# Performance work log

Hardware: AMD Instinct MI355X
Metric: run time of the kernel (lower is better)

The kernel has to match this reference:

```python
import jax, jax.numpy as jnp
import numpy as np

B, T, D = 64, 512, 512
K_CODES = 256
K_FUTURE = 2


def _gru(x, w_ih, w_hh, b_ih, b_hh):
    # x: [B,T,D]; PyTorch GRU gate order: r, z, n; weights [3D, D]
    xg = jnp.einsum('btd,gd->btg', x, w_ih) + b_ih  # [B,T,3D] precomputed input gates

    def step(h, xg_t):
        hg = h @ w_hh.T + b_hh                      # [B,3D]
        xr, xz, xn = jnp.split(xg_t, 3, axis=-1)
        hr, hz, hn = jnp.split(hg, 3, axis=-1)
        r = jax.nn.sigmoid(xr + hr)
        z = jax.nn.sigmoid(xz + hz)
        n = jnp.tanh(xn + r * hn)
        h_new = (1.0 - z) * n + z * h
        return h_new, h_new

    h0 = jnp.zeros((x.shape[0], w_hh.shape[1]), x.dtype)
    _, hs = jax.lax.scan(step, h0, jnp.swapaxes(xg, 0, 1))
    return jnp.swapaxes(hs, 0, 1)  # [B,T,D]


def setup_inputs() -> dict:
    key = jax.random.key(0)
    ks = jax.random.split(key, 8)
    return {
        'features': jax.random.normal(ks[0], (B, T, D), jnp.float32),
        'codebook': jax.random.uniform(ks[1], (K_CODES, D), jnp.float32, -0.1, 0.1),
        'w_ih': jax.random.normal(ks[2], (3 * D, D), jnp.float32) * 0.02,
        'w_hh': jax.random.normal(ks[3], (3 * D, D), jnp.float32) * 0.02,
        'b_ih': jax.random.normal(ks[4], (3 * D,), jnp.float32) * 0.02,
        'b_hh': jax.random.normal(ks[5], (3 * D,), jnp.float32) * 0.02,
        'proj_w': jax.random.normal(ks[6], (D, D), jnp.float32) * 0.02,
        'proj_b': jax.random.normal(ks[7], (D,), jnp.float32) * 0.02,
    }


def reference(features, codebook, w_ih, w_hh, b_ih, b_hh, proj_w, proj_b):
    b, t, d = features.shape
    # --- quantize: cdist + argmin + gather (squared dists give same argmin) ---
    flat = features.reshape(-1, d)                              # [B*T, D]
    d2 = (jnp.sum(flat * flat, axis=1, keepdims=True)
          - 2.0 * flat @ codebook.T
          + jnp.sum(codebook * codebook, axis=1))               # [B*T, K]
    indices = jnp.argmin(d2, axis=1)                            # [B*T]
    quantized = codebook[indices].reshape(b, t, d)              # gather
    indices = indices.reshape(b, t)

    # --- context prediction loss ---
    hidden = _gru(quantized, w_ih, w_hh, b_ih, b_hh)            # [B,T,D]
    context_proj = hidden @ proj_w.T + proj_b                   # [B,T,D]
    k_max = min(K_FUTURE, t - 1)
    cp_loss = jnp.float32(0.0)
    for k in range(1, k_max + 1):
        cp_loss = cp_loss + jnp.mean((context_proj[:, :-k] - features[:, k:]) ** 2)
    cp_loss = cp_loss / k_max

    # --- VQ loss (stop_gradient mirrors torch .detach()) ---
    commitment_loss = jnp.mean((jax.lax.stop_gradient(features) - quantized) ** 2)
    codebook_loss = jnp.mean((features - jax.lax.stop_gradient(quantized)) ** 2)
    vq_loss = commitment_loss + 0.25 * codebook_loss

    total_loss = cp_loss + vq_loss
    return quantized, indices, total_loss, cp_loss, vq_loss
```

## Files before the change

### kernel.cpp

```cpp
#include <hip/hip_runtime.h>
#include <hip/hip_bf16.h>

#define B_ 64
#define T_ 512
#define D_ 512
#define K_ 256
#define G3 1536

typedef __attribute__((ext_vector_type(8))) short sh8;
typedef __attribute__((ext_vector_type(4))) short sh4;
typedef __attribute__((ext_vector_type(4))) float fx4;
typedef __attribute__((ext_vector_type(4))) int   ix4;

__device__ __forceinline__ short f2bf(float x) {
  __hip_bfloat16 h = __float2bfloat16(x);
  union { __hip_bfloat16 h; short s; } u; u.h = h; return u.s;
}
__device__ __forceinline__ float sigm(float x) { return 1.f / (1.f + __expf(-x)); }
__device__ __forceinline__ float tanh_fast(float x) {
  float e2 = __expf(-2.f * x);
  return (1.f - e2) / (1.f + e2);
}

__global__ void k_cnorm(const float* __restrict__ cb, double* __restrict__ cn) {
  int c = threadIdx.x;
  if (c < K_) {
    double s = 0.0;
    for (int k = 0; k < D_; ++k) { double v = cb[c * D_ + k]; s += v * v; }
    cn[c] = s;
  }
}

__global__ __launch_bounds__(256) void k_cg(const float* __restrict__ cb,
                                            const float* __restrict__ wih,
                                            const float* __restrict__ bih,
                                            const float* __restrict__ bhh,
                                            float* __restrict__ cg) {
  __shared__ float wl[16][512];
  int j0 = blockIdx.x * 16, c0 = blockIdx.y * 64;
  for (int v = threadIdx.x; v < 16 * 128; v += 256) {
    int r = v >> 7, q = v & 127;
    *(fx4*)&wl[r][q * 4] = *(const fx4*)&wih[(j0 + r) * D_ + q * 4];
  }
  __syncthreads();
  for (int p = threadIdx.x; p < 1024; p += 256) {
    int j = p >> 6, c = c0 + (p & 63);
    fx4 a = {0.f, 0.f, 0.f, 0.f};
    const float* cbr = &cb[c * D_];
    for (int q = 0; q < 128; ++q) {
      fx4 w4 = *(fx4*)&wl[j][q * 4];
      fx4 c4 = *(const fx4*)&cbr[q * 4];
      a += w4 * c4;
    }
    int jg = j0 + j;
    float bias = bih[jg] + (jg < 1024 ? bhh[jg] : 0.f);
    cg[c * G3 + jg] = ((a.x + a.y) + (a.z + a.w)) + bias;
  }
}

__global__ void k_cvt(const float* __restrict__ src, __hip_bfloat16* __restrict__ dst, int n4) {
  int i = blockIdx.x * blockDim.x + threadIdx.x;
  if (i < n4) {
    fx4 v = *(const fx4*)&src[i * 4];
    sh4 o; o[0] = f2bf(v.x); o[1] = f2bf(v.y); o[2] = f2bf(v.z); o[3] = f2bf(v.w);
    *(sh4*)&dst[i * 4] = o;
  }
}

__global__ __launch_bounds__(256) void k_quant(const float* __restrict__ feat,
                                               const float* __restrict__ cb,
                                               const double* __restrict__ cn,
                                               int* __restrict__ idxw,
                                               float* __restrict__ outq,
                                               float* __restrict__ outi,
                                               double* __restrict__ lacc) {
  __shared__ float fl[16][516];
  __shared__ double ss1[16][16], ss2[16][16];
  __shared__ int ii1[16][16], ii2[16][16];
  __shared__ int idxl[16];
  __shared__ float rsv[4];
  int row0 = blockIdx.x * 16;
  int tid = threadIdx.x;
  for (int v = tid; v < 16 * 128; v += 256) {
    int r = v >> 7, q = v & 127;
    *(fx4*)&fl[r][q * 4] = *(const fx4*)&feat[(row0 + r) * D_ + q * 4];
  }
  __syncthreads();
  int r = tid & 15, g = tid >> 4;
  fx4 acc[16];
#pragma unroll
  for (int c = 0; c < 16; ++c) acc[c] = (fx4){0.f, 0.f, 0.f, 0.f};
  for (int ch = 0; ch < 8; ++ch) {
    fx4 fc[16];
#pragma unroll
    for (int q = 0; q < 16; ++q) fc[q] = *(fx4*)&fl[r][ch * 64 + q * 4];
#pragma unroll
    for (int c = 0; c < 16; ++c) {
      const float* cbp = &cb[(g * 16 + c) * D_ + ch * 64];
#pragma unroll
      for (int q = 0; q < 16; ++q) {
        fx4 c4 = *(const fx4*)&cbp[q * 4];
        acc[c] += fc[q] * c4;
      }
    }
  }
  double b1 = 1e300, b2 = 1e300; int i1 = 0, i2 = 0;
#pragma unroll
  for (int c = 0; c < 16; ++c) {
    int ci = g * 16 + c;
    double dot = (double)acc[c].x + acc[c].y + acc[c].z + acc[c].w;
    double s = cn[ci] - 2.0 * dot;
    if (s < b1) { b2 = b1; i2 = i1; b1 = s; i1 = ci; }
    else if (s < b2) { b2 = s; i2 = ci; }
  }
  ss1[r][g] = b1; ss2[r][g] = b2; ii1[r][g] = i1; ii2[r][g] = i2;
  __syncthreads();
  if (tid < 16) {
    int rr = tid;
    double c1 = 1e300, c2 = 1e300; int j1 = 0, j2 = 0;
    for (int g2 = 0; g2 < 16; ++g2) {
      double s = ss1[rr][g2]; int ix = ii1[rr][g2];
      if (s < c1 || (s == c1 && ix < j1)) { c2 = c1; j2 = j1; c1 = s; j1 = ix; }
      else if (s < c2 || (s == c2 && ix < j2)) { c2 = s; j2 = ix; }
      s = ss2[rr][g2]; ix = ii2[rr][g2];
      if (s < c1 || (s == c1 && ix < j1)) { c2 = c1; j2 = j1; c1 = s; j1 = ix; }
      else if (s < c2 || (s == c2 && ix < j2)) { c2 = s; j2 = ix; }
    }
    int pick = j1;
    if (c2 - c1 < 1e-4) {
      double d1 = 0.0, d2 = 0.0;
      for (int k = 0; k < D_; ++k) {
        double fv = fl[rr][k];
        d1 += fv * (double)cb[j1 * D_ + k];
        d2 += fv * (double)cb[j2 * D_ + k];
      }
      double e1 = cn[j1] - 2.0 * d1, e2 = cn[j2] - 2.0 * d2;
      if (e2 < e1 || (e2 == e1 && j2 < j1)) pick = j2;
    }
    idxl[rr] = pick;
    idxw[row0 + rr] = pick;
    outi[row0 + rr] = (float)pick;
  }
  __syncthreads();
  float vs = 0.f;
  for (int v = tid; v < 16 * 128; v += 256) {
    int rr = v >> 7, q = v & 127;
    fx4 c4 = *(const fx4*)&cb[idxl[rr] * D_ + q * 4];
    *(fx4*)&outq[(row0 + rr) * D_ + q * 4] = c4;
    fx4 f4 = *(fx4*)&fl[rr][q * 4];
    fx4 d = f4 - c4;
    vs += d.x * d.x + d.y * d.y + d.z * d.z + d.w * d.w;
  }
#pragma unroll
  for (int off = 32; off > 0; off >>= 1) vs += __shfl_down(vs, off);
  if ((tid & 63) == 0) rsv[tid >> 6] = vs;
  __syncthreads();
  if (tid == 0) atomicAdd(&lacc[2], (double)(rsv[0] + rsv[1] + rsv[2] + rsv[3]));
}

__global__ __launch_bounds__(256, 1) void k_gru(const float* __restrict__ whh,
                                                const float* __restrict__ bhh,
                                                const float* __restrict__ cg,
                                                const int* __restrict__ idx,
                                                __hip_bfloat16* __restrict__ hid,
                                                unsigned int* __restrict__ flag,
                                                int* __restrict__ xcca,
                                                unsigned int* __restrict__ bar0) {
  int bid = blockIdx.x;
  int g = bid & 7, s = bid >> 3;
  int tid = threadIdx.x;
  int w = tid >> 6, lane = tid & 63, l15 = lane & 15, l4 = lane >> 4;
  int wv = s * 4 + w;

  sh8 A0[16], A1[16], A2[16];
#pragma unroll
  for (int kt = 0; kt < 16; ++kt) {
#pragma unroll
    for (int t3 = 0; t3 < 3; ++t3) {
      const float* wr = &whh[((t3 * 512) + s * 64 + w * 16 + l15) * D_];
      int k0 = kt * 32 + l4 * 8;
      fx4 x = *(const fx4*)&wr[k0];
      fx4 y = *(const fx4*)&wr[k0 + 4];
      sh8 tt;
      tt[0] = f2bf(x.x); tt[1] = f2bf(x.y); tt[2] = f2bf(x.z); tt[3] = f2bf(x.w);
      tt[4] = f2bf(y.x); tt[5] = f2bf(y.y); tt[6] = f2bf(y.z); tt[7] = f2bf(y.w);
      if (t3 == 0) A0[kt] = tt; else if (t3 == 1) A1[kt] = tt; else A2[kt] = tt;
    }
  }

  const bool act = (l15 < 8);
  const int b = l15 & 7;
  const int dg0 = s * 64 + w * 16 + l4 * 4;

  fx4 bn = *(const fx4*)&bhh[1024 + dg0];
  fx4 hp = {0.f, 0.f, 0.f, 0.f};

  __shared__ int sh_fast;
  if (tid == 0) {
    int xcc = 0;
    asm volatile("s_getreg_b32 %0, hwreg(HW_REG_XCC_ID)" : "=s"(xcc));
    __hip_atomic_store(&xcca[bid], xcc, __ATOMIC_RELEASE, __HIP_MEMORY_SCOPE_AGENT);
    __hip_atomic_fetch_add(bar0, 1u, __ATOMIC_ACQ_REL, __HIP_MEMORY_SCOPE_AGENT);
    while (__hip_atomic_load(bar0, __ATOMIC_ACQUIRE, __HIP_MEMORY_SCOPE_AGENT) < 64u)
      __builtin_amdgcn_s_sleep(2);
    int x0 = __hip_atomic_load(&xcca[g], __ATOMIC_RELAXED, __HIP_MEMORY_SCOPE_AGENT);
    int f = 1;
    for (int m = 1; m < 8; ++m)
      if (__hip_atomic_load(&xcca[g + 8 * m], __ATOMIC_RELAXED, __HIP_MEMORY_SCOPE_AGENT) != x0)
        f = 0;
    sh_fast = f;
    __threadfence();
  }
  __syncthreads();
  const bool fast = (sh_fast != 0);

  const unsigned* myfp = &flag[(g * 32 + (lane & 31)) * 32];

  for (int t = 0; t < T_; ++t) {
    fx4 cr = {0, 0, 0, 0}, cz = {0, 0, 0, 0}, cnn = {0, 0, 0, 0};
    if (act) {
      int ci = idx[(g * 8 + b) * T_ + t];
      const float* cgr = &cg[(size_t)ci * G3 + dg0];
      cr  = *(const fx4*)cgr;
      cz  = *(const fx4*)(cgr + 512);
      cnn = *(const fx4*)(cgr + 1024);
    }

    fx4 a0 = {0, 0, 0, 0}, a1 = {0, 0, 0, 0}, a2 = {0, 0, 0, 0};
    if (t > 0) {
      for (;;) {
        unsigned v = __hip_atomic_load(myfp, __ATOMIC_RELAXED, __HIP_MEMORY_SCOPE_AGENT);
        if (__all((int)(v >= (unsigned)t))) break;
        __builtin_amdgcn_s_sleep(1);
      }
      asm volatile("" ::: "memory");
      if (!fast) __threadfence();

      const __hip_bfloat16* hrow =
          &hid[((size_t)(g * 8 + b) * T_ + (t - 1)) * D_];
#pragma unroll
      for (int kt = 0; kt < 16; ++kt) {
        sh8 bfr = {0, 0, 0, 0, 0, 0, 0, 0};
        if (act) bfr = *(const sh8*)&hrow[kt * 32 + l4 * 8];
        a0 = __builtin_amdgcn_mfma_f32_16x16x32_bf16(A0[kt], bfr, a0, 0, 0, 0);
        a1 = __builtin_amdgcn_mfma_f32_16x16x32_bf16(A1[kt], bfr, a1, 0, 0, 0);
        a2 = __builtin_amdgcn_mfma_f32_16x16x32_bf16(A2[kt], bfr, a2, 0, 0, 0);
      }
    }

    if (act) {
      sh4 hb4;
#pragma unroll
      for (int rg = 0; rg < 4; ++rg) {
        float rr = sigm(cr[rg] + a0[rg]);
        float zz = sigm(cz[rg] + a1[rg]);
        float nn = tanh_fast(cnn[rg] + rr * (a2[rg] + bn[rg]));
        float hv = (1.f - zz) * nn + zz * hp[rg];
        hp[rg] = hv;
        hb4[rg] = f2bf(hv);
      }
      *(sh4*)&hid[((size_t)(g * 8 + b) * T_ + t) * D_ + dg0] = hb4;
    }
    asm volatile("s_waitcnt vmcnt(0)" ::: "memory");
    if (!fast) __threadfence();
    if (lane == 0)
      __hip_atomic_store(&flag[(g * 32 + wv) * 32], (unsigned)(t + 1),
                         __ATOMIC_RELAXED, __HIP_MEMORY_SCOPE_AGENT);
  }
}

__global__ __launch_bounds__(256) void k_proj(const __hip_bfloat16* __restrict__ hid,
                                              const __hip_bfloat16* __restrict__ pwb,
                                              const float* __restrict__ pb,
                                              const float* __restrict__ feat,
                                              double* __restrict__ lacc) {
  __shared__ char Bl[512 * 64];
  __shared__ char Al[32 * 64];
  __shared__ float rs1[4], rs2[4];
  int Mb = blockIdx.x * 32;
  int tid = threadIdx.x;
  int w = tid >> 6, lane = tid & 63, l15 = lane & 15, l4 = lane >> 4;
  fx4 acc[2][8];
#pragma unroll
  for (int a = 0; a < 2; ++a)
#pragma unroll
    for (int b = 0; b < 8; ++b) acc[a][b] = (fx4){0, 0, 0, 0};

  for (int kc = 0; kc < 16; ++kc) {
    for (int v = tid; v < 2048; v += 256) {
      int rw = v >> 2, sg = v & 3;
      ix4 d = *(const ix4*)&pwb[rw * D_ + kc * 32 + sg * 8];
      *(ix4*)(Bl + rw * 64 + ((sg * 16) ^ ((rw & 7) << 4))) = d;
    }
    if (tid < 128) {
      int rw = tid >> 2, sg = tid & 3;
      ix4 d = *(const ix4*)&hid[(size_t)(Mb + rw) * D_ + kc * 32 + sg * 8];
      *(ix4*)(Al + rw * 64 + ((sg * 16) ^ ((rw & 7) << 4))) = d;
    }
    __syncthreads();
    sh8 af0, af1;
    {
      int m = l15;
      af0 = *(const sh8*)(Al + m * 64 + ((l4 * 16) ^ ((m & 7) << 4)));
      m = 16 + l15;
      af1 = *(const sh8*)(Al + m * 64 + ((l4 * 16) ^ ((m & 7) << 4)));
    }
#pragma unroll
    for (int nt = 0; nt < 8; ++nt) {
      int n = (w * 8 + nt) * 16 + l15;
      sh8 bf = *(const sh8*)(Bl + n * 64 + ((l4 * 16) ^ ((n & 7) << 4)));
      acc[0][nt] = __builtin_amdgcn_mfma_f32_16x16x32_bf16(af0, bf, acc[0][nt], 0, 0, 0);
      acc[1][nt] = __builtin_amdgcn_mfma_f32_16x16x32_bf16(af1, bf, acc[1][nt], 0, 0, 0);
    }
    __syncthreads();
  }

  float s1 = 0.f, s2 = 0.f;
#pragma unroll
  for (int mt = 0; mt < 2; ++mt) {
#pragma unroll
    for (int nt = 0; nt < 8; ++nt) {
      int n = (w * 8 + nt) * 16 + l15;
      float bias = pb[n];
#pragma unroll
      for (int rg = 0; rg < 4; ++rg) {
        int m = Mb + mt * 16 + l4 * 4 + rg;
        float val = acc[mt][nt][rg] + bias;
        int t = m & (T_ - 1);
        if (t < T_ - 1) { float d = val - feat[(size_t)(m + 1) * D_ + n]; s1 += d * d; }
        if (t < T_ - 2) { float d = val - feat[(size_t)(m + 2) * D_ + n]; s2 += d * d; }
      }
    }
  }
#pragma unroll
  for (int off = 32; off > 0; off >>= 1) {
    s1 += __shfl_down(s1, off);
    s2 += __shfl_down(s2, off);
  }
  if (lane == 0) { rs1[w] = s1; rs2[w] = s2; }
  __syncthreads();
  if (tid == 0) {
    atomicAdd(&lacc[0], (double)rs1[0] + rs1[1] + rs1[2] + rs1[3]);
    atomicAdd(&lacc[1], (double)rs2[0] + rs2[1] + rs2[2] + rs2[3]);
  }
}

__global__ void k_fin(const double* __restrict__ lacc, float* __restrict__ outl) {
  if (threadIdx.x == 0) {
    double cp = 0.5 * (lacc[0] / ((double)B_ * (T_ - 1) * D_) +
                       lacc[1] / ((double)B_ * (T_ - 2) * D_));
    double vq = 1.25 * lacc[2] / ((double)B_ * T_ * D_);
    outl[0] = (float)(cp + vq);
    outl[1] = (float)cp;
    outl[2] = (float)vq;
  }
}

extern "C" void kernel_launch(void* const* d_in, const int* in_sizes, int n_in,
                              void* d_out, int out_size, void* d_ws, size_t ws_size,
                              hipStream_t stream) {
  (void)in_sizes; (void)n_in; (void)out_size; (void)ws_size;
  const float* feat = (const float*)d_in[0];
  const float* cb   = (const float*)d_in[1];
  const float* wih  = (const float*)d_in[2];
  const float* whh  = (const float*)d_in[3];
  const float* bih  = (const float*)d_in[4];
  const float* bhh  = (const float*)d_in[5];
  const float* pw   = (const float*)d_in[6];
  const float* pb   = (const float*)d_in[7];

  float* out  = (float*)d_out;
  float* outq = out;
  float* outi = out + (size_t)B_ * T_ * D_;
  float* outl = outi + B_ * T_;

  char* ws = (char*)d_ws;
  size_t o = 0;
  auto alloc = [&](size_t sz) { void* p = ws + o; o += (sz + 255) & ~(size_t)255; return p; };
  float*          cg   = (float*)alloc(sizeof(float) * K_ * G3);
  double*         cn   = (double*)alloc(sizeof(double) * K_);
  int*            idxw = (int*)alloc(sizeof(int) * B_ * T_);
  __hip_bfloat16* pwb  = (__hip_bfloat16*)alloc(sizeof(__hip_bfloat16) * D_ * D_);
  double*         lacc = (double*)alloc(sizeof(double) * 4);
  unsigned*       flag = (unsigned*)alloc(sizeof(unsigned) * 256 * 32);
  int*            xcca = (int*)alloc(sizeof(int) * 64);
  unsigned*       bar0 = (unsigned*)alloc(sizeof(unsigned) * 4);
  __hip_bfloat16* hid  = (__hip_bfloat16*)alloc(sizeof(__hip_bfloat16) * (size_t)B_ * T_ * D_);

  hipMemsetAsync(lacc, 0, sizeof(double) * 4, stream);
  hipMemsetAsync(flag, 0, sizeof(unsigned) * 256 * 32, stream);
  hipMemsetAsync(xcca, 0, sizeof(int) * 64, stream);
  hipMemsetAsync(bar0, 0, sizeof(unsigned) * 4, stream);

  hipLaunchKernelGGL(k_cnorm, dim3(1), dim3(256), 0, stream, cb, cn);
  hipLaunchKernelGGL(k_cg, dim3(96, 4), dim3(256), 0, stream, cb, wih, bih, bhh, cg);
  hipLaunchKernelGGL(k_cvt, dim3(256), dim3(256), 0, stream, pw, pwb, D_ * D_ / 4);
  hipLaunchKernelGGL(k_quant, dim3(2048), dim3(256), 0, stream, feat, cb, cn, idxw, outq, outi, lacc);
  hipLaunchKernelGGL(k_gru, dim3(64), dim3(256), 0, stream, whh, bhh, cg, idxw, hid, flag, xcca, bar0);
  hipLaunchKernelGGL(k_proj, dim3(1024), dim3(256), 0, stream, hid, pwb, pb, feat, lacc);
  hipLaunchKernelGGL(k_fin, dim3(1), dim3(64), 0, stream, lacc, outl);
}
```

Before: 3.293 ms.

## Pack GRU step flags contiguously, raise wave priority, add MFMA spinner blocks

The per-wave step flags are no longer padded to one word every 32; each group's 32 flags now share one contiguous region, so a poll can fetch them in one coalesced load. GRU waves get raised scheduling priority. The grid also grows by 184 dummy blocks that issue back-to-back MFMAs on zeros until the 64 real blocks signal completion through a new done counter, apparently to hold the device in a high clock or power state. The trade-off is that packed flags put all writers of a group on the same cache line, and the spinner blocks burn power and occupy CUs while the recurrence runs.

```diff
diff --git a/kernel.cpp b/kernel.cpp
--- a/kernel.cpp
+++ b/kernel.cpp
@@ -165,10 +165,25 @@
                                                 __hip_bfloat16* __restrict__ hid,
                                                 unsigned int* __restrict__ flag,
                                                 int* __restrict__ xcca,
-                                                unsigned int* __restrict__ bar0) {
+                                                unsigned int* __restrict__ bar0,
+                                                unsigned int* __restrict__ done) {
   int bid = blockIdx.x;
+  int tid = threadIdx.x;
+
+  if (bid >= 64) {
+    fx4 hacc = {0.f, 0.f, 0.f, 0.f};
+    sh8 hz = {0, 0, 0, 0, 0, 0, 0, 0};
+    while (__hip_atomic_load(done, __ATOMIC_RELAXED, __HIP_MEMORY_SCOPE_AGENT) < 64u) {
+#pragma unroll 8
+      for (int i = 0; i < 2048; ++i)
+        hacc = __builtin_amdgcn_mfma_f32_16x16x32_bf16(hz, hz, hacc, 0, 0, 0);
+    }
+    asm volatile("" :: "v"(hacc[0]));
+    return;
+  }
+
+  __builtin_amdgcn_s_setprio(1);
   int g = bid & 7, s = bid >> 3;
-  int tid = threadIdx.x;
   int w = tid >> 6, lane = tid & 63, l15 = lane & 15, l4 = lane >> 4;
   int wv = s * 4 + w;
 
@@ -214,7 +229,7 @@
   __syncthreads();
   const bool fast = (sh_fast != 0);
 
-  const unsigned* myfp = &flag[(g * 32 + (lane & 31)) * 32];
+  const unsigned* pollp = &flag[g * 32 + (lane & 31)];
 
   for (int t = 0; t < T_; ++t) {
     fx4 cr = {0, 0, 0, 0}, cz = {0, 0, 0, 0}, cnn = {0, 0, 0, 0};
@@ -229,7 +244,7 @@
     fx4 a0 = {0, 0, 0, 0}, a1 = {0, 0, 0, 0}, a2 = {0, 0, 0, 0};
     if (t > 0) {
       for (;;) {
-        unsigned v = __hip_atomic_load(myfp, __ATOMIC_RELAXED, __HIP_MEMORY_SCOPE_AGENT);
+        unsigned v = __hip_atomic_load(pollp, __ATOMIC_RELAXED, __HIP_MEMORY_SCOPE_AGENT);
         if (__all((int)(v >= (unsigned)t))) break;
         __builtin_amdgcn_s_sleep(1);
       }
@@ -264,9 +279,13 @@
     asm volatile("s_waitcnt vmcnt(0)" ::: "memory");
     if (!fast) __threadfence();
     if (lane == 0)
-      __hip_atomic_store(&flag[(g * 32 + wv) * 32], (unsigned)(t + 1),
+      __hip_atomic_store(&flag[g * 32 + wv], (unsigned)(t + 1),
                          __ATOMIC_RELAXED, __HIP_MEMORY_SCOPE_AGENT);
   }
+
+  __syncthreads();
+  if (tid == 0)
+    __hip_atomic_fetch_add(done, 1u, __ATOMIC_RELEASE, __HIP_MEMORY_SCOPE_AGENT);
 }
 
 __global__ __launch_bounds__(256) void k_proj(const __hip_bfloat16* __restrict__ hid,
@@ -382,21 +401,23 @@
   int*            idxw = (int*)alloc(sizeof(int) * B_ * T_);
   __hip_bfloat16* pwb  = (__hip_bfloat16*)alloc(sizeof(__hip_bfloat16) * D_ * D_);
   double*         lacc = (double*)alloc(sizeof(double) * 4);
-  unsigned*       flag = (unsigned*)alloc(sizeof(unsigned) * 256 * 32);
+  unsigned*       flag = (unsigned*)alloc(sizeof(unsigned) * 256);
   int*            xcca = (int*)alloc(sizeof(int) * 64);
   unsigned*       bar0 = (unsigned*)alloc(sizeof(unsigned) * 4);
+  unsigned*       dn   = (unsigned*)alloc(sizeof(unsigned) * 4);
   __hip_bfloat16* hid  = (__hip_bfloat16*)alloc(sizeof(__hip_bfloat16) * (size_t)B_ * T_ * D_);
 
   hipMemsetAsync(lacc, 0, sizeof(double) * 4, stream);
-  hipMemsetAsync(flag, 0, sizeof(unsigned) * 256 * 32, stream);
+  hipMemsetAsync(flag, 0, sizeof(unsigned) * 256, stream);
   hipMemsetAsync(xcca, 0, sizeof(int) * 64, stream);
   hipMemsetAsync(bar0, 0, sizeof(unsigned) * 4, stream);
+  hipMemsetAsync(dn,   0, sizeof(unsigned) * 4, stream);
 
   hipLaunchKernelGGL(k_cnorm, dim3(1), dim3(256), 0, stream, cb, cn);
   hipLaunchKernelGGL(k_cg, dim3(96, 4), dim3(256), 0, stream, cb, wih, bih, bhh, cg);
   hipLaunchKernelGGL(k_cvt, dim3(256), dim3(256), 0, stream, pw, pwb, D_ * D_ / 4);
   hipLaunchKernelGGL(k_quant, dim3(2048), dim3(256), 0, stream, feat, cb, cn, idxw, outq, outi, lacc);
-  hipLaunchKernelGGL(k_gru, dim3(64), dim3(256), 0, stream, whh, bhh, cg, idxw, hid, flag, xcca, bar0);
+  hipLaunchKernelGGL(k_gru, dim3(248), dim3(256), 0, stream, whh, bhh, cg, idxw, hid, flag, xcca, bar0, dn);
   hipLaunchKernelGGL(k_proj, dim3(1024), dim3(256), 0, stream, hid, pwb, pb, feat, lacc);
   hipLaunchKernelGGL(k_fin, dim3(1), dim3(64), 0, stream, lacc, outl);
 }
```

Result: slower. 3.446 ms (+4.6%).
